# Optimization experiments

Measured on AMD Instinct MI355X. Metric: run time of the kernel, lower is better.

Reference implementation:

```python
import jax, jax.numpy as jnp
import numpy as np

D = 2048  # filter_dim
B = 4096  # tokens per TTT step


def setup_inputs() -> dict:
    key = jax.random.key(0)
    ks = jax.random.split(key, 8)
    s = 1.0 / np.sqrt(D)  # kaiming-ish scale so activations stay O(1)
    return {
        "src": jax.random.normal(ks[0], (B, D), jnp.float32),
        "theta_k": jax.random.normal(ks[1], (D, D), jnp.float32) * s,
        "theta_q": jax.random.normal(ks[2], (D, D), jnp.float32) * s,
        "theta_v": jax.random.normal(ks[3], (D, D), jnp.float32) * s,
        "W": jax.random.normal(ks[4], (D, D), jnp.float32) * s,
        "b": jnp.zeros((D,), jnp.float32),
        "lr_w": jax.random.uniform(ks[5], (D, D), jnp.float32) * 0.1,
        "lr_b": jax.random.uniform(ks[6], (D,), jnp.float32) * 0.1,
    }


def reference(src, theta_k, theta_q, theta_v, W, b, lr_w, lr_b):
    # Projections: src is [B, D], thetas are [D, D]
    train_view = src @ theta_k           # [B, D]
    label_view = src @ theta_v           # [B, D]
    test_view = src @ theta_q            # [B, D]

    target = label_view - train_view     # reconstruction target
    pred = train_view @ W.T + b          # nn.Linear(train_view)
    err = pred - target                  # [B, D]

    # Analytic grads of MSELoss (mean over B*D elements) wrt W ([D,D]) and b ([D])
    n = err.size  # B * D (static)
    coef = 2.0 / n
    gW = coef * (err.T @ train_view)     # [D, D], matches w.weight layout
    gb = coef * jnp.sum(err, axis=0)     # [D]

    # Per-element learning-rate SGD step (the in-place parameter rewrite)
    W_new = W - lr_w * gW
    b_new = b - lr_b * gb

    # Query with updated weights + residual
    z = test_view @ W_new.T + b_new + test_view
    return z
```

## Files before the change

### kernel.cpp

```cpp
#include <hip/hip_runtime.h>
#include <hip/hip_bf16.h>
#include <hip/hip_fp8.h>
#include <stdint.h>

#define D_DIM 2048
#define B_TOK 4096
#define COEF (2.0f / 8388608.0f)

typedef __bf16 bf16x8 __attribute__((ext_vector_type(8)));
typedef float  f32x4  __attribute__((ext_vector_type(4)));
typedef int    i32x8  __attribute__((ext_vector_type(8)));
typedef unsigned short u16x8 __attribute__((ext_vector_type(8)));

__device__ __forceinline__ unsigned short f2bf(float f) {
  return __builtin_bit_cast(unsigned short, (__bf16)f);
}
__device__ __forceinline__ float bf2f(unsigned short u) {
  return (float)__builtin_bit_cast(__bf16, u);
}
__device__ __forceinline__ unsigned char f2f8(float f) {
  __hip_fp8_e4m3 v(f);
  return v.__x;
}

__device__ __forceinline__ void async16(const void* g, void* l) {
  __builtin_amdgcn_global_load_lds(
      (__attribute__((address_space(1))) void*)(g),
      (__attribute__((address_space(3))) void*)(l),
      16, 0, 0);
}

__device__ __forceinline__ void gemm_core(const unsigned short* __restrict__ Ablk,
                                          const unsigned short* __restrict__ Bblk,
                                          const int lda, const int ldb, const int KC,
                                          unsigned short* As, unsigned short* Bs,
                                          f32x4 acc[4][4]) {
  const int tid  = threadIdx.x;
  const int lane = tid & 63;
  const int wv   = tid >> 6;
  const int wm   = wv & 1, wn = wv >> 1;
  const int t    = lane & 15;
  const int quad = lane >> 4;
  const int lrow = lane >> 3;
  const int kq   = lane & 7;
  const int kqs  = kq ^ lrow;

  const int nk = KC >> 6;
  for (int kt = 0; kt < nk; ++kt) {
    const int k0 = kt << 6;
#pragma unroll
    for (int l = 0; l < 4; ++l) {
      const int seg = wv * 4 + l;
      const int r   = seg * 8 + lrow;
      async16(Ablk + (size_t)r * lda + k0 + kqs * 8, As + seg * 512);
      async16(Bblk + (size_t)r * ldb + k0 + kqs * 8, Bs + seg * 512);
    }
    __syncthreads();
#pragma unroll
    for (int s = 0; s < 2; ++s) {
      bf16x8 af[4], bfr[4];
#pragma unroll
      for (int i = 0; i < 4; ++i) {
        const int rm = wm * 64 + i * 16 + t;
        af[i]  = *(const bf16x8*)(As + rm * 64 + (((s << 2) + quad) ^ (rm & 7)) * 8);
        const int rn = wn * 64 + i * 16 + t;
        bfr[i] = *(const bf16x8*)(Bs + rn * 64 + (((s << 2) + quad) ^ (rn & 7)) * 8);
      }
#pragma unroll
      for (int i = 0; i < 4; ++i)
#pragma unroll
        for (int j = 0; j < 4; ++j)
          acc[i][j] = __builtin_amdgcn_mfma_f32_16x16x32_bf16(af[i], bfr[j], acc[i][j], 0, 0, 0);
    }
    __syncthreads();
  }
}

#define GEMM_PROLOGUE(AP, BP, LDAv, LDBv, KCv)                                 \
  __shared__ __align__(16) unsigned short As[128 * 64];                        \
  __shared__ __align__(16) unsigned short Bs[128 * 64];                        \
  const unsigned short* Ablk = (AP) + (size_t)blockIdx.y * 128 * (LDAv);       \
  const unsigned short* Bblk = (BP) + (size_t)blockIdx.x * 128 * (LDBv);       \
  f32x4 acc[4][4];                                                             \
  _Pragma("unroll") for (int i = 0; i < 4; ++i)                                \
  _Pragma("unroll") for (int j = 0; j < 4; ++j)                                \
      acc[i][j] = (f32x4){0.f, 0.f, 0.f, 0.f};                                 \
  gemm_core(Ablk, Bblk, (LDAv), (LDBv), (KCv), As, Bs, acc);                   \
  const int lane = threadIdx.x & 63;                                           \
  const int wv = threadIdx.x >> 6;                                             \
  const int wm = wv & 1, wn = wv >> 1;                                         \
  const int t = lane & 15, quad = lane >> 4;                                   \
  const int gm_base = blockIdx.y * 128 + wm * 64;                              \
  const int gn_base = blockIdx.x * 128 + wn * 64;

__device__ __forceinline__ void gemm_core_f8(const unsigned char* __restrict__ Ablk,
                                             const unsigned char* __restrict__ Bblk,
                                             const int lda, const int ldb, const int KC,
                                             unsigned char* As, unsigned char* Bs,
                                             f32x4 acc[4][4]) {
  const int tid  = threadIdx.x;
  const int lane = tid & 63;
  const int wv   = tid >> 6;
  const int wm   = wv & 1, wn = wv >> 1;
  const int t    = lane & 15;
  const int quad = lane >> 4;
  const int lrow = lane >> 3;
  const int kq   = lane & 7;
  const int kqs  = kq ^ lrow;

  const int nk = KC >> 7;
  for (int kt = 0; kt < nk; ++kt) {
    const int k0 = kt << 7;
#pragma unroll
    for (int l = 0; l < 4; ++l) {
      const int seg = wv * 4 + l;
      const int r   = seg * 8 + lrow;
      async16(Ablk + (size_t)r * lda + k0 + kqs * 16, As + seg * 1024);
      async16(Bblk + (size_t)r * ldb + k0 + kqs * 16, Bs + seg * 1024);
    }
    __syncthreads();
    i32x8 af[4];
#pragma unroll
    for (int i = 0; i < 4; ++i) {
      const int rm = wm * 64 + i * 16 + t;
      const unsigned char* base = As + rm * 128;
      const int x = rm & 7;
      const uint4 lo = *(const uint4*)(base + (((quad << 1)    ) ^ x) * 16);
      const uint4 hi = *(const uint4*)(base + (((quad << 1) | 1) ^ x) * 16);
      af[i] = (i32x8){(int)lo.x, (int)lo.y, (int)lo.z, (int)lo.w,
                      (int)hi.x, (int)hi.y, (int)hi.z, (int)hi.w};
    }
#pragma unroll
    for (int j = 0; j < 4; ++j) {
      const int rn = wn * 64 + j * 16 + t;
      const unsigned char* base = Bs + rn * 128;
      const int x = rn & 7;
      const uint4 lo = *(const uint4*)(base + (((quad << 1)    ) ^ x) * 16);
      const uint4 hi = *(const uint4*)(base + (((quad << 1) | 1) ^ x) * 16);
      const i32x8 bq = (i32x8){(int)lo.x, (int)lo.y, (int)lo.z, (int)lo.w,
                               (int)hi.x, (int)hi.y, (int)hi.z, (int)hi.w};
#pragma unroll
      for (int i = 0; i < 4; ++i)
        acc[i][j] = __builtin_amdgcn_mfma_scale_f32_16x16x128_f8f6f4(
            af[i], bq, acc[i][j], 0, 0, 0, 127, 0, 127);
    }
    __syncthreads();
  }
}

#define GEMM8_PROLOGUE(AP, BP, LDAv, LDBv, KCv)                                \
  __shared__ __align__(16) unsigned char As8[128 * 128];                       \
  __shared__ __align__(16) unsigned char Bs8[128 * 128];                       \
  const unsigned char* Ablk = (AP) + (size_t)blockIdx.y * 128 * (LDAv);        \
  const unsigned char* Bblk = (BP) + (size_t)blockIdx.x * 128 * (LDBv);        \
  f32x4 acc[4][4];                                                             \
  _Pragma("unroll") for (int i = 0; i < 4; ++i)                                \
  _Pragma("unroll") for (int j = 0; j < 4; ++j)                                \
      acc[i][j] = (f32x4){0.f, 0.f, 0.f, 0.f};                                 \
  gemm_core_f8(Ablk, Bblk, (LDAv), (LDBv), (KCv), As8, Bs8, acc);              \
  const int lane = threadIdx.x & 63;                                           \
  const int wv = threadIdx.x >> 6;                                             \
  const int wm = wv & 1, wn = wv >> 1;                                         \
  const int t = lane & 15, quad = lane >> 4;                                   \
  const int gm_base = blockIdx.y * 128 + wm * 64;                              \
  const int gn_base = blockIdx.x * 128 + wn * 64;

__global__ __launch_bounds__(256) void gemm_train_f8(
    const unsigned char* __restrict__ srcA,
    const unsigned char* __restrict__ thkT8,
    unsigned char* __restrict__ src_cat_f8,
    unsigned char* __restrict__ trainT8) {
  GEMM8_PROLOGUE(srcA, thkT8, 4096, 2048, 2048)
  unsigned char* scr = ((wv >> 1) ? Bs8 : As8) + (wv & 1) * 2304;
#pragma unroll
  for (int p = 0; p < 2; ++p) {
#pragma unroll
    for (int jl = 0; jl < 2; ++jl) {
      const int j = p * 2 + jl;
      const int gn = gn_base + j * 16 + t;
#pragma unroll
      for (int i = 0; i < 4; ++i) {
        const int gm0 = gm_base + i * 16 + quad * 4;
        uchar4 pk = make_uchar4(f2f8(acc[i][j][0]), f2f8(acc[i][j][1]),
                                f2f8(acc[i][j][2]), f2f8(acc[i][j][3]));
        src_cat_f8[(size_t)(gm0 + 0) * 4096 + gn] = pk.x;
        src_cat_f8[(size_t)(gm0 + 1) * 4096 + gn] = pk.y;
        src_cat_f8[(size_t)(gm0 + 2) * 4096 + gn] = pk.z;
        src_cat_f8[(size_t)(gm0 + 3) * 4096 + gn] = pk.w;
        *(uchar4*)(scr + (jl * 16 + t) * 72 + i * 16 + quad * 4) = pk;
      }
    }
    __syncthreads();
    const int row = lane >> 3, chunk = lane & 7;
#pragma unroll
    for (int q = 0; q < 4; ++q) {
      const int rr = q * 8 + row;
      const uint2 v = *(const uint2*)(scr + rr * 72 + chunk * 8);
      *(uint2*)(trainT8 + (size_t)(gn_base + p * 32 + rr) * B_TOK + gm_base + chunk * 8) = v;
    }
    __syncthreads();
  }
}

__global__ __launch_bounds__(256) void gemm_test(
    const unsigned short* __restrict__ src_bf,
    const unsigned short* __restrict__ thqT,
    unsigned short* __restrict__ testv) {
  GEMM_PROLOGUE(src_bf, thqT, 2048, 2048, 2048)
#pragma unroll
  for (int i = 0; i < 4; ++i) {
#pragma unroll
    for (int j = 0; j < 4; ++j) {
      const int gm0 = gm_base + i * 16 + quad * 4;
      const int gn  = gn_base + j * 16 + t;
#pragma unroll
      for (int r = 0; r < 4; ++r)
        testv[(size_t)(gm0 + r) * D_DIM + gn] = f2bf(acc[i][j][r]);
    }
  }
}

__global__ __launch_bounds__(256) void gemm_err_f8(
    const unsigned char* __restrict__ src_cat_f8,
    const unsigned char* __restrict__ Wcat_f8,
    const float* __restrict__ bvec,
    unsigned char* __restrict__ errT8,
    float* __restrict__ gb) {
  GEMM8_PROLOGUE(src_cat_f8, Wcat_f8, 4096, 4096, 4096)
  unsigned char* scr = ((wv >> 1) ? Bs8 : As8) + (wv & 1) * 2304;
#pragma unroll
  for (int p = 0; p < 2; ++p) {
#pragma unroll
    for (int jl = 0; jl < 2; ++jl) {
      const int j = p * 2 + jl;
      const int gn = gn_base + j * 16 + t;
      const float bias = bvec[gn];
      float cs = 0.f;
#pragma unroll
      for (int i = 0; i < 4; ++i) {
        const float e0 = acc[i][j][0] + bias, e1 = acc[i][j][1] + bias;
        const float e2 = acc[i][j][2] + bias, e3 = acc[i][j][3] + bias;
        *(uchar4*)(scr + (jl * 16 + t) * 72 + i * 16 + quad * 4) =
            make_uchar4(f2f8(e0), f2f8(e1), f2f8(e2), f2f8(e3));
        cs += e0 + e1 + e2 + e3;
      }
      cs += __shfl_xor(cs, 16);
      cs += __shfl_xor(cs, 32);
      if (quad == 0) atomicAdd(&gb[gn], cs);
    }
    __syncthreads();
    const int row = lane >> 3, chunk = lane & 7;
#pragma unroll
    for (int q = 0; q < 4; ++q) {
      const int rr = q * 8 + row;
      const uint2 v = *(const uint2*)(scr + rr * 72 + chunk * 8);
      *(uint2*)(errT8 + (size_t)(gn_base + p * 32 + rr) * B_TOK + gm_base + chunk * 8) = v;
    }
    __syncthreads();
  }
}

__global__ __launch_bounds__(256) void gemm_gw_f8(
    const unsigned char* __restrict__ errT8,
    const unsigned char* __restrict__ trainT8,
    float* __restrict__ P0, float* __restrict__ P1) {
  const int z = blockIdx.z;
  const unsigned char* Abase = errT8 + z * 2048;
  const unsigned char* Bbase = trainT8 + z * 2048;
  GEMM8_PROLOGUE(Abase, Bbase, B_TOK, B_TOK, 2048)
  float* P = (z == 0) ? P0 : P1;
#pragma unroll
  for (int i = 0; i < 4; ++i) {
#pragma unroll
    for (int j = 0; j < 4; ++j) {
      const int gm0 = gm_base + i * 16 + quad * 4;
      const int gn  = gn_base + j * 16 + t;
#pragma unroll
      for (int r = 0; r < 4; ++r)
        P[(size_t)(gm0 + r) * D_DIM + gn] = acc[i][j][r];
    }
  }
}

__global__ __launch_bounds__(256) void wnew_reduce(
    const float* __restrict__ P0, const float* __restrict__ P1,
    const float* __restrict__ W, const float* __restrict__ lr_w,
    unsigned short* __restrict__ Wnew) {
  const int i = blockIdx.x * 256 + threadIdx.x;
  const float4 p0 = ((const float4*)P0)[i];
  const float4 p1 = ((const float4*)P1)[i];
  const float4 w  = ((const float4*)W)[i];
  const float4 l  = ((const float4*)lr_w)[i];
  ((ushort4*)Wnew)[i] = make_ushort4(
      f2bf(w.x - l.x * (COEF * (p0.x + p1.x))),
      f2bf(w.y - l.y * (COEF * (p0.y + p1.y))),
      f2bf(w.z - l.z * (COEF * (p0.z + p1.z))),
      f2bf(w.w - l.w * (COEF * (p0.w + p1.w))));
}

__global__ __launch_bounds__(256) void gemm_out(
    const unsigned short* __restrict__ testv,
    const unsigned short* __restrict__ Wnew,
    const float* __restrict__ bvec,
    const float* __restrict__ lr_b,
    const float* __restrict__ gb,
    float* __restrict__ out) {
  GEMM_PROLOGUE(testv, Wnew, 2048, 2048, 2048)
#pragma unroll
  for (int j = 0; j < 4; ++j) {
    const int gn = gn_base + j * 16 + t;
    const float bias = bvec[gn] - lr_b[gn] * (COEF * gb[gn]);
#pragma unroll
    for (int i = 0; i < 4; ++i) {
      const int gm0 = gm_base + i * 16 + quad * 4;
#pragma unroll
      for (int r = 0; r < 4; ++r) {
        const size_t idx = (size_t)(gm0 + r) * D_DIM + gn;
        out[idx] = acc[i][j][r] + bias + bf2f(testv[idx]);
      }
    }
  }
}

__global__ __launch_bounds__(256) void cvt_all(const float* __restrict__ src,
                                               const float* __restrict__ W,
                                               unsigned short* __restrict__ src_bf,
                                               unsigned char* __restrict__ src_cat_f8,
                                               unsigned char* __restrict__ Wcat_f8,
                                               float* __restrict__ gb) {
  const int i = blockIdx.x * 256 + threadIdx.x;
  if (i < 512) ((float4*)gb)[i] = (float4){0.f, 0.f, 0.f, 0.f};
  if (i < 2097152) {
    const int m = i >> 9, c = i & 511;
    const float4 v = ((const float4*)src)[i];
    ((ushort4*)src_bf)[i] = make_ushort4(f2bf(v.x), f2bf(v.y), f2bf(v.z), f2bf(v.w));
    *(uchar4*)(src_cat_f8 + (size_t)m * 4096 + 2048 + c * 4) =
        make_uchar4(f2f8(v.x), f2f8(v.y), f2f8(v.z), f2f8(v.w));
  } else {
    const int j = i - 2097152;
    const int n = j >> 9, c = j & 511;
    const float4 v = ((const float4*)W)[j];
    *(uchar4*)(Wcat_f8 + (size_t)n * 4096 + c * 4) =
        make_uchar4(f2f8(v.x), f2f8(v.y), f2f8(v.z), f2f8(v.w));
  }
}

__global__ __launch_bounds__(256) void tcvt(
    const float* __restrict__ thk, const float* __restrict__ thq,
    const float* __restrict__ thv,
    unsigned char* __restrict__ thkT8, unsigned short* __restrict__ thqT,
    unsigned char* __restrict__ Wcat_f8) {
  __shared__ float tile[32][33];
  const int z = blockIdx.z;
  const int bx = blockIdx.x * 32, by = blockIdx.y * 32;
  const int tx = threadIdx.x & 31, ty = threadIdx.x >> 5;
#pragma unroll
  for (int l = 0; l < 4; ++l) {
    const int r = ty + l * 8;
    const size_t idx = (size_t)(by + r) * D_DIM + bx + tx;
    tile[r][tx] = (z == 0) ? thk[idx] : (z == 1) ? thq[idx] : (thk[idx] - thv[idx]);
  }
  __syncthreads();
#pragma unroll
  for (int l = 0; l < 4; ++l) {
    const int r = ty + l * 8;
    if (z == 0)
      thkT8[(size_t)(bx + r) * 2048 + by + tx] = f2f8(tile[tx][r]);
    else if (z == 1)
      thqT[(size_t)(bx + r) * 2048 + by + tx] = f2bf(tile[tx][r]);
    else
      Wcat_f8[(size_t)(bx + r) * 4096 + 2048 + by + tx] = f2f8(tile[tx][r]);
  }
}

extern "C" void kernel_launch(void* const* d_in, const int* in_sizes, int n_in,
                              void* d_out, int out_size, void* d_ws, size_t ws_size,
                              hipStream_t stream) {
  const float* src = (const float*)d_in[0];
  const float* thk = (const float*)d_in[1];
  const float* thq = (const float*)d_in[2];
  const float* thv = (const float*)d_in[3];
  const float* W   = (const float*)d_in[4];
  const float* bv  = (const float*)d_in[5];
  const float* lrw = (const float*)d_in[6];
  const float* lrb = (const float*)d_in[7];
  float* out = (float*)d_out;

  char* ws = (char*)d_ws;
  const size_t MB = 1024 * 1024;
  unsigned short* src_bf     = (unsigned short*)(ws + 0);
  unsigned char*  src_cat_f8 = (unsigned char*)(ws + 16 * MB);
  unsigned char*  Wcat_f8    = (unsigned char*)(ws + 32 * MB);
  unsigned char*  thkT8      = (unsigned char*)(ws + 40 * MB);
  unsigned short* thqT       = (unsigned short*)(ws + 44 * MB);
  unsigned char*  trainT8    = (unsigned char*)(ws + 52 * MB);
  unsigned short* testv      = (unsigned short*)(ws + 60 * MB);
  unsigned char*  errT8      = (unsigned char*)(ws + 76 * MB);
  unsigned short* WnewBf     = (unsigned short*)(ws + 84 * MB);
  float*          P0         = (float*)(ws + 92 * MB);
  float*          P1         = (float*)(ws + 108 * MB);
  float*          gb         = (float*)(ws + 124 * MB);

  cvt_all<<<12288, 256, 0, stream>>>(src, W, src_bf, src_cat_f8, Wcat_f8, gb);
  tcvt<<<dim3(64, 64, 3), 256, 0, stream>>>(thk, thq, thv, thkT8, thqT, Wcat_f8);

  gemm_train_f8<<<dim3(16, 32), 256, 0, stream>>>(src_cat_f8 + 2048, thkT8,
                                                  src_cat_f8, trainT8);
  gemm_test<<<dim3(16, 32), 256, 0, stream>>>(src_bf, thqT, testv);
  gemm_err_f8<<<dim3(16, 32), 256, 0, stream>>>(src_cat_f8, Wcat_f8, bv, errT8, gb);
  gemm_gw_f8<<<dim3(16, 16, 2), 256, 0, stream>>>(errT8, trainT8, P0, P1);
  wnew_reduce<<<4096, 256, 0, stream>>>(P0, P1, W, lrw, WnewBf);
  gemm_out<<<dim3(16, 32), 256, 0, stream>>>(testv, WnewBf, bv, lrb, gb, out);
}
```

Measured before the change: 350.4 us.

## Double-buffer LDS tiles in bf16 and fp8 GEMM cores to overlap loads

Both GEMM main loops now use two LDS buffers. The next K-tile is issued with async global-to-LDS copies into one buffer while MFMAs read the current tile from the other, replacing the load-barrier-compute-barrier sequence. This is meant to hide global memory latency behind matrix math. In exchange, shared memory per block doubles to 64KB, which can lower occupancy, and the barrier at the end of each iteration still waits for the prefetch to land.

```diff
diff --git a/kernel.cpp b/kernel.cpp
--- a/kernel.cpp
+++ b/kernel.cpp
@@ -46,25 +46,35 @@
   const int kqs  = kq ^ lrow;
 
   const int nk = KC >> 6;
-  for (int kt = 0; kt < nk; ++kt) {
-    const int k0 = kt << 6;
+
+  auto stage = [&](int buf, int k0) {
+    unsigned short* Ad = As + buf * 8192;
+    unsigned short* Bd = Bs + buf * 8192;
 #pragma unroll
     for (int l = 0; l < 4; ++l) {
       const int seg = wv * 4 + l;
       const int r   = seg * 8 + lrow;
-      async16(Ablk + (size_t)r * lda + k0 + kqs * 8, As + seg * 512);
-      async16(Bblk + (size_t)r * ldb + k0 + kqs * 8, Bs + seg * 512);
-    }
-    __syncthreads();
+      async16(Ablk + (size_t)r * lda + k0 + kqs * 8, Ad + seg * 512);
+      async16(Bblk + (size_t)r * ldb + k0 + kqs * 8, Bd + seg * 512);
+    }
+  };
+
+  stage(0, 0);
+  __syncthreads();
+  for (int kt = 0; kt < nk; ++kt) {
+    const int cur = kt & 1;
+    if (kt + 1 < nk) stage(cur ^ 1, (kt + 1) << 6);
+    const unsigned short* Ac = As + cur * 8192;
+    const unsigned short* Bc = Bs + cur * 8192;
 #pragma unroll
     for (int s = 0; s < 2; ++s) {
       bf16x8 af[4], bfr[4];
 #pragma unroll
       for (int i = 0; i < 4; ++i) {
         const int rm = wm * 64 + i * 16 + t;
-        af[i]  = *(const bf16x8*)(As + rm * 64 + (((s << 2) + quad) ^ (rm & 7)) * 8);
+        af[i]  = *(const bf16x8*)(Ac + rm * 64 + (((s << 2) + quad) ^ (rm & 7)) * 8);
         const int rn = wn * 64 + i * 16 + t;
-        bfr[i] = *(const bf16x8*)(Bs + rn * 64 + (((s << 2) + quad) ^ (rn & 7)) * 8);
+        bfr[i] = *(const bf16x8*)(Bc + rn * 64 + (((s << 2) + quad) ^ (rn & 7)) * 8);
       }
 #pragma unroll
       for (int i = 0; i < 4; ++i)
@@ -77,8 +87,8 @@
 }
 
 #define GEMM_PROLOGUE(AP, BP, LDAv, LDBv, KCv)                                 \
-  __shared__ __align__(16) unsigned short As[128 * 64];                        \
-  __shared__ __align__(16) unsigned short Bs[128 * 64];                        \
+  __shared__ __align__(16) unsigned short As[2 * 128 * 64];                    \
+  __shared__ __align__(16) unsigned short Bs[2 * 128 * 64];                    \
   const unsigned short* Ablk = (AP) + (size_t)blockIdx.y * 128 * (LDAv);       \
   const unsigned short* Bblk = (BP) + (size_t)blockIdx.x * 128 * (LDBv);       \
   f32x4 acc[4][4];                                                             \
@@ -109,21 +119,31 @@
   const int kqs  = kq ^ lrow;
 
   const int nk = KC >> 7;
-  for (int kt = 0; kt < nk; ++kt) {
-    const int k0 = kt << 7;
+
+  auto stage = [&](int buf, int k0) {
+    unsigned char* Ad = As + buf * 16384;
+    unsigned char* Bd = Bs + buf * 16384;
 #pragma unroll
     for (int l = 0; l < 4; ++l) {
       const int seg = wv * 4 + l;
       const int r   = seg * 8 + lrow;
-      async16(Ablk + (size_t)r * lda + k0 + kqs * 16, As + seg * 1024);
-      async16(Bblk + (size_t)r * ldb + k0 + kqs * 16, Bs + seg * 1024);
-    }
-    __syncthreads();
+      async16(Ablk + (size_t)r * lda + k0 + kqs * 16, Ad + seg * 1024);
+      async16(Bblk + (size_t)r * ldb + k0 + kqs * 16, Bd + seg * 1024);
+    }
+  };
+
+  stage(0, 0);
+  __syncthreads();
+  for (int kt = 0; kt < nk; ++kt) {
+    const int cur = kt & 1;
+    if (kt + 1 < nk) stage(cur ^ 1, (kt + 1) << 7);
+    const unsigned char* Ac = As + cur * 16384;
+    const unsigned char* Bc = Bs + cur * 16384;
     i32x8 af[4];
 #pragma unroll
     for (int i = 0; i < 4; ++i) {
       const int rm = wm * 64 + i * 16 + t;
-      const unsigned char* base = As + rm * 128;
+      const unsigned char* base = Ac + rm * 128;
       const int x = rm & 7;
       const uint4 lo = *(const uint4*)(base + (((quad << 1)    ) ^ x) * 16);
       const uint4 hi = *(const uint4*)(base + (((quad << 1) | 1) ^ x) * 16);
@@ -133,7 +153,7 @@
 #pragma unroll
     for (int j = 0; j < 4; ++j) {
       const int rn = wn * 64 + j * 16 + t;
-      const unsigned char* base = Bs + rn * 128;
+      const unsigned char* base = Bc + rn * 128;
       const int x = rn & 7;
       const uint4 lo = *(const uint4*)(base + (((quad << 1)    ) ^ x) * 16);
       const uint4 hi = *(const uint4*)(base + (((quad << 1) | 1) ^ x) * 16);
@@ -149,8 +169,8 @@
 }
 
 #define GEMM8_PROLOGUE(AP, BP, LDAv, LDBv, KCv)                                \
-  __shared__ __align__(16) unsigned char As8[128 * 128];                       \
-  __shared__ __align__(16) unsigned char Bs8[128 * 128];                       \
+  __shared__ __align__(16) unsigned char As8[2 * 128 * 128];                   \
+  __shared__ __align__(16) unsigned char Bs8[2 * 128 * 128];                   \
   const unsigned char* Ablk = (AP) + (size_t)blockIdx.y * 128 * (LDAv);        \
   const unsigned char* Bblk = (BP) + (size_t)blockIdx.x * 128 * (LDBv);        \
   f32x4 acc[4][4];                                                             \
```

Result: slower. 360.2 us (+2.8%).

## Triple-buffer bf16 GEMMs with 256x128 tiles, 512 threads and block swizzle

Applied to the files above, without the earlier changes.

Replaces the bf16 GEMM core used by the test-view and output GEMMs with a 256x128 tile run by 8 waves. A triple-buffered LDS pipeline issues async global-to-LDS loads two k-steps ahead and waits with a vmcnt count instead of two full __syncthreads per step. It also adds a grouped block-index swizzle for L2 reuse and raises wave priority around the MFMA bursts. This is meant to hide global load latency and cut barrier overhead, at the cost of 144KB of LDS per block and fewer blocks in flight.

```diff
diff --git a/kernel.cpp b/kernel.cpp
--- a/kernel.cpp
+++ b/kernel.cpp
@@ -30,15 +30,16 @@
       16, 0, 0);
 }
 
-__device__ __forceinline__ void gemm_core(const unsigned short* __restrict__ Ablk,
-                                          const unsigned short* __restrict__ Bblk,
-                                          const int lda, const int ldb, const int KC,
-                                          unsigned short* As, unsigned short* Bs,
-                                          f32x4 acc[4][4]) {
+__device__ __forceinline__ void gemm_core_256(const unsigned short* __restrict__ Ablk,
+                                              const unsigned short* __restrict__ Bblk,
+                                              const int lda, const int ldb, const int KC,
+                                              unsigned short* As, unsigned short* Bs,
+                                              f32x4 acc[4][4]) {
   const int tid  = threadIdx.x;
   const int lane = tid & 63;
   const int wv   = tid >> 6;
-  const int wm   = wv & 1, wn = wv >> 1;
+  const int wm   = wv >> 1;
+  const int wn   = wv & 1;
   const int t    = lane & 15;
   const int quad = lane >> 4;
   const int lrow = lane >> 3;
@@ -46,52 +47,79 @@
   const int kqs  = kq ^ lrow;
 
   const int nk = KC >> 6;
-  for (int kt = 0; kt < nk; ++kt) {
+
+  auto stage = [&](int buf, int kt) {
     const int k0 = kt << 6;
+    unsigned short* Ad = As + buf * 16384;
+    unsigned short* Bd = Bs + buf * 8192;
 #pragma unroll
     for (int l = 0; l < 4; ++l) {
       const int seg = wv * 4 + l;
       const int r   = seg * 8 + lrow;
-      async16(Ablk + (size_t)r * lda + k0 + kqs * 8, As + seg * 512);
-      async16(Bblk + (size_t)r * ldb + k0 + kqs * 8, Bs + seg * 512);
-    }
-    __syncthreads();
+      async16(Ablk + (size_t)r * lda + k0 + kqs * 8, Ad + seg * 512);
+    }
+#pragma unroll
+    for (int l = 0; l < 2; ++l) {
+      const int seg = wv * 2 + l;
+      const int r   = seg * 8 + lrow;
+      async16(Bblk + (size_t)r * ldb + k0 + kqs * 8, Bd + seg * 512);
+    }
+  };
+
+  stage(0, 0);
+  if (nk > 1) stage(1, 1);
+  int cur = 0, nxt = 2;
+  for (int kt = 0; kt < nk; ++kt) {
+    if (kt + 1 < nk) asm volatile("s_waitcnt vmcnt(6)" ::: "memory");
+    else             asm volatile("s_waitcnt vmcnt(0)" ::: "memory");
+    __builtin_amdgcn_s_barrier();
+    __builtin_amdgcn_sched_barrier(0);
+    if (kt + 2 < nk) stage(nxt, kt + 2);
+    __builtin_amdgcn_sched_barrier(0);
+    const unsigned short* Ac = As + cur * 16384;
+    const unsigned short* Bc = Bs + cur * 8192;
 #pragma unroll
     for (int s = 0; s < 2; ++s) {
       bf16x8 af[4], bfr[4];
 #pragma unroll
       for (int i = 0; i < 4; ++i) {
         const int rm = wm * 64 + i * 16 + t;
-        af[i]  = *(const bf16x8*)(As + rm * 64 + (((s << 2) + quad) ^ (rm & 7)) * 8);
+        af[i]  = *(const bf16x8*)(Ac + rm * 64 + (((s << 2) + quad) ^ (rm & 7)) * 8);
         const int rn = wn * 64 + i * 16 + t;
-        bfr[i] = *(const bf16x8*)(Bs + rn * 64 + (((s << 2) + quad) ^ (rn & 7)) * 8);
+        bfr[i] = *(const bf16x8*)(Bc + rn * 64 + (((s << 2) + quad) ^ (rn & 7)) * 8);
       }
+      __builtin_amdgcn_s_setprio(1);
 #pragma unroll
       for (int i = 0; i < 4; ++i)
 #pragma unroll
         for (int j = 0; j < 4; ++j)
           acc[i][j] = __builtin_amdgcn_mfma_f32_16x16x32_bf16(af[i], bfr[j], acc[i][j], 0, 0, 0);
-    }
-    __syncthreads();
-  }
-}
-
-#define GEMM_PROLOGUE(AP, BP, LDAv, LDBv, KCv)                                 \
-  __shared__ __align__(16) unsigned short As[128 * 64];                        \
-  __shared__ __align__(16) unsigned short Bs[128 * 64];                        \
-  const unsigned short* Ablk = (AP) + (size_t)blockIdx.y * 128 * (LDAv);       \
-  const unsigned short* Bblk = (BP) + (size_t)blockIdx.x * 128 * (LDBv);       \
+      __builtin_amdgcn_s_setprio(0);
+    }
+    cur = (cur == 2) ? 0 : cur + 1;
+    nxt = (nxt == 2) ? 0 : nxt + 1;
+  }
+}
+
+#define GEMM_PROLOGUE256(AP, BP, LDAv, LDBv, KCv)                              \
+  __shared__ __align__(16) unsigned short As[3 * 16384];                       \
+  __shared__ __align__(16) unsigned short Bs[3 * 8192];                        \
+  const int lin = blockIdx.y * 16 + blockIdx.x;                                \
+  const int swz = (lin & 7) * 32 + (lin >> 3);                                 \
+  const int bx = swz & 15, by = swz >> 4;                                      \
+  const unsigned short* Ablk = (AP) + (size_t)by * 256 * (LDAv);               \
+  const unsigned short* Bblk = (BP) + (size_t)bx * 128 * (LDBv);               \
   f32x4 acc[4][4];                                                             \
   _Pragma("unroll") for (int i = 0; i < 4; ++i)                                \
   _Pragma("unroll") for (int j = 0; j < 4; ++j)                                \
       acc[i][j] = (f32x4){0.f, 0.f, 0.f, 0.f};                                 \
-  gemm_core(Ablk, Bblk, (LDAv), (LDBv), (KCv), As, Bs, acc);                   \
+  gemm_core_256(Ablk, Bblk, (LDAv), (LDBv), (KCv), As, Bs, acc);               \
   const int lane = threadIdx.x & 63;                                           \
   const int wv = threadIdx.x >> 6;                                             \
-  const int wm = wv & 1, wn = wv >> 1;                                         \
+  const int wm = wv >> 1, wn = wv & 1;                                         \
   const int t = lane & 15, quad = lane >> 4;                                   \
-  const int gm_base = blockIdx.y * 128 + wm * 64;                              \
-  const int gn_base = blockIdx.x * 128 + wn * 64;
+  const int gm_base = by * 256 + wm * 64;                                      \
+  const int gn_base = bx * 128 + wn * 64;
 
 __device__ __forceinline__ void gemm_core_f8(const unsigned char* __restrict__ Ablk,
                                              const unsigned char* __restrict__ Bblk,
@@ -202,11 +230,11 @@
   }
 }
 
-__global__ __launch_bounds__(256) void gemm_test(
+__global__ __launch_bounds__(512, 2) void gemm_test(
     const unsigned short* __restrict__ src_bf,
     const unsigned short* __restrict__ thqT,
     unsigned short* __restrict__ testv) {
-  GEMM_PROLOGUE(src_bf, thqT, 2048, 2048, 2048)
+  GEMM_PROLOGUE256(src_bf, thqT, 2048, 2048, 2048)
 #pragma unroll
   for (int i = 0; i < 4; ++i) {
 #pragma unroll
@@ -298,14 +326,14 @@
       f2bf(w.w - l.w * (COEF * (p0.w + p1.w))));
 }
 
-__global__ __launch_bounds__(256) void gemm_out(
+__global__ __launch_bounds__(512, 2) void gemm_out(
     const unsigned short* __restrict__ testv,
     const unsigned short* __restrict__ Wnew,
     const float* __restrict__ bvec,
     const float* __restrict__ lr_b,
     const float* __restrict__ gb,
     float* __restrict__ out) {
-  GEMM_PROLOGUE(testv, Wnew, 2048, 2048, 2048)
+  GEMM_PROLOGUE256(testv, Wnew, 2048, 2048, 2048)
 #pragma unroll
   for (int j = 0; j < 4; ++j) {
     const int gn = gn_base + j * 16 + t;
@@ -406,9 +434,9 @@
 
   gemm_train_f8<<<dim3(16, 32), 256, 0, stream>>>(src_cat_f8 + 2048, thkT8,
                                                   src_cat_f8, trainT8);
-  gemm_test<<<dim3(16, 32), 256, 0, stream>>>(src_bf, thqT, testv);
+  gemm_test<<<dim3(16, 16), 512, 0, stream>>>(src_bf, thqT, testv);
   gemm_err_f8<<<dim3(16, 32), 256, 0, stream>>>(src_cat_f8, Wcat_f8, bv, errT8, gb);
   gemm_gw_f8<<<dim3(16, 16, 2), 256, 0, stream>>>(errT8, trainT8, P0, P1);
   wnew_reduce<<<4096, 256, 0, stream>>>(P0, P1, W, lrw, WnewBf);
-  gemm_out<<<dim3(16, 32), 256, 0, stream>>>(testv, WnewBf, bv, lrb, gb, out);
-}
+  gemm_out<<<dim3(16, 16), 512, 0, stream>>>(testv, WnewBf, bv, lrb, gb, out);
+}
```

New measurement: 357.6 us. +2.1%, slower.
